# Kernel optimization log

Hardware: AMD Instinct MI355X
Metric: run time of the kernel (lower is better)

Reference implementation:

```python
import jax, jax.numpy as jnp
import numpy as np

BATCH, SEQ, STATE, D_IN, D_OUT = 32, 8192, 128, 128, 128


def setup_inputs() -> dict:
    key = jax.random.key(0)
    k1, k2, k3, k4, k5 = jax.random.split(key, 5)
    A = jnp.tril(jax.random.normal(k1, (STATE, STATE), dtype=jnp.float32) * 0.01)
    B = jax.random.normal(k2, (STATE, D_IN), dtype=jnp.float32) * 0.01
    C = jax.random.normal(k3, (D_OUT, STATE), dtype=jnp.float32) * 0.01
    D = jax.random.normal(k4, (D_OUT, D_IN), dtype=jnp.float32) * 0.01
    u = jax.random.normal(k5, (BATCH, SEQ, D_IN), dtype=jnp.float32)
    return {"u": u, "A": A, "B": B, "C": C, "D": D}


def reference(u, A, B, C, D):
    # u: [b, L, d_in]; A: [S, S] (lower-tri); B: [S, d_in]; C: [d_out, S]; D: [d_out, d_in]
    S = A.shape[0]
    Bu = jnp.einsum('bld,sd->bls', u, B)                      # [b, L, S]
    I_minus_A = jnp.eye(S, dtype=u.dtype) - A                 # [S, S], lower-tri
    # Solve (I - A) x = Bu^T. The matrix is shared across batch and time, so
    # fold (b, L) into one rhs-column axis: one trsm instead of b batched solves.
    rhs = Bu.reshape(-1, S).T                                 # [S, b*L]
    x = jax.scipy.linalg.solve_triangular(I_minus_A, rhs, lower=True)  # [S, b*L]
    x_seq = x.T.reshape(Bu.shape)                             # [b, L, S]
    y = jnp.einsum('bls,os->blo', x_seq, C) + jnp.einsum('bld,od->blo', u, D)
    return y
```

## Files before the change

### kernel.cpp

```cpp
#include <hip/hip_runtime.h>
#include <stdint.h>

typedef __attribute__((ext_vector_type(8))) short bf16x8;
typedef __attribute__((ext_vector_type(4))) float f32x4;

static __device__ __forceinline__ uint16_t f2bf(float f) {
    uint32_t u;
    __builtin_memcpy(&u, &f, 4);
    return (uint16_t)((u + 0x7FFFu + ((u >> 16) & 1u)) >> 16);
}

__global__ __launch_bounds__(128) void k1_solve(const float* __restrict__ Ag,
                                                const float* __restrict__ Bg,
                                                float* __restrict__ X) {
    __shared__ float As[128 * 128];
    const int d = threadIdx.x;
    for (int i = 0; i < 128; ++i) As[i * 128 + d] = Ag[i * 128 + d];
    __syncthreads();

    float x[128];
#pragma unroll
    for (int s = 0; s < 128; ++s) {
        const float* Ar = &As[s * 128];
        float a0 = 0.f, a1 = 0.f, a2 = 0.f, a3 = 0.f;
        const int s4 = s & ~3;
#pragma unroll
        for (int t = 0; t < s4; t += 4) {
            a0 += Ar[t + 0] * x[t + 0];
            a1 += Ar[t + 1] * x[t + 1];
            a2 += Ar[t + 2] * x[t + 2];
            a3 += Ar[t + 3] * x[t + 3];
        }
#pragma unroll
        for (int t = s4; t < s; ++t) a0 += Ar[t] * x[t];
        float num = Bg[s * 128 + d] + ((a0 + a1) + (a2 + a3));
        x[s] = num / (1.0f - Ar[s]);
    }
#pragma unroll
    for (int s = 0; s < 128; ++s) X[s * 128 + d] = x[s];
}

__global__ __launch_bounds__(128) void k2_makeM(const float* __restrict__ X,
                                                const float* __restrict__ Cg,
                                                const float* __restrict__ Dg,
                                                uint16_t* __restrict__ Mfrag) {
    const int o = blockIdx.x;
    const int d = threadIdx.x;
    float a0 = 0.f, a1 = 0.f, a2 = 0.f, a3 = 0.f;
#pragma unroll
    for (int s = 0; s < 128; s += 4) {
        a0 += Cg[o * 128 + s + 0] * X[(s + 0) * 128 + d];
        a1 += Cg[o * 128 + s + 1] * X[(s + 1) * 128 + d];
        a2 += Cg[o * 128 + s + 2] * X[(s + 2) * 128 + d];
        a3 += Cg[o * 128 + s + 3] * X[(s + 3) * 128 + d];
    }
    float m = ((a0 + a1) + (a2 + a3)) + Dg[o * 128 + d];

    const int c = o >> 4, n = o & 15;
    const int t = d >> 5, r = d & 31;
    const int half = r >> 3, j = r & 7;
    const int lane = half * 16 + n;
    const int f = c * 4 + t;
    Mfrag[(f * 64 + lane) * 8 + j] = f2bf(m);
}

__global__ __launch_bounds__(256, 2) void k3_gemm(const float* __restrict__ U,
                                                  const uint16_t* __restrict__ Mfrag,
                                                  float* __restrict__ Y) {
    const int lane = threadIdx.x & 63;
    const int wid  = threadIdx.x >> 6;

    bf16x8 Bfr[8][4];
#pragma unroll
    for (int c = 0; c < 8; ++c)
#pragma unroll
        for (int t = 0; t < 4; ++t)
            Bfr[c][t] = *reinterpret_cast<const bf16x8*>(Mfrag + ((c * 4 + t) * 64 + lane) * 8);

    const int am = lane & 15;
    const int kh = lane >> 4;

#pragma unroll 1
    for (int it = 0; it < 4; ++it) {
        const int rowbase = blockIdx.x * 256 + it * 64 + wid * 16;

        const float* up = U + (size_t)(rowbase + am) * 128 + kh * 8;
        bf16x8 Afr[4];
#pragma unroll
        for (int t = 0; t < 4; ++t) {
            f32x4 lo = *reinterpret_cast<const f32x4*>(up + t * 32);
            f32x4 hi = *reinterpret_cast<const f32x4*>(up + t * 32 + 4);
            bf16x8 a;
#pragma unroll
            for (int j = 0; j < 4; ++j) {
                a[j]     = (short)f2bf(lo[j]);
                a[4 + j] = (short)f2bf(hi[j]);
            }
            Afr[t] = a;
        }

        f32x4 acc[8] = {};
#pragma unroll
        for (int c = 0; c < 8; ++c)
#pragma unroll
            for (int t = 0; t < 4; ++t)
                acc[c] = __builtin_amdgcn_mfma_f32_16x16x32_bf16(Afr[t], Bfr[c][t], acc[c], 0, 0, 0);

        float* yp = Y + (size_t)(rowbase + kh * 4) * 128 + am;
#pragma unroll
        for (int c = 0; c < 8; ++c)
#pragma unroll
            for (int r = 0; r < 4; ++r)
                yp[(size_t)r * 128 + c * 16] = acc[c][r];
    }
}

extern "C" void kernel_launch(void* const* d_in, const int* in_sizes, int n_in,
                              void* d_out, int out_size, void* d_ws, size_t ws_size,
                              hipStream_t stream) {
    const float* u = (const float*)d_in[0];
    const float* A = (const float*)d_in[1];
    const float* B = (const float*)d_in[2];
    const float* C = (const float*)d_in[3];
    const float* D = (const float*)d_in[4];

    float*    X     = (float*)d_ws;
    uint16_t* Mfrag = (uint16_t*)((char*)d_ws + 65536);
    float*    Y     = (float*)d_out;

    hipLaunchKernelGGL(k1_solve, dim3(1),    dim3(128), 0, stream, A, B, X);
    hipLaunchKernelGGL(k2_makeM, dim3(128),  dim3(128), 0, stream, X, C, D, Mfrag);
    hipLaunchKernelGGL(k3_gemm,  dim3(1024), dim3(256), 0, stream, u, Mfrag, Y);
}
```

Measured before the change: 305.6 us.

## Stage M fragments in LDS and raise GEMM occupancy with more blocks

Measured after the change: 302.6 us. About the same (-1.0%).

```diff
diff --git a/kernel.cpp b/kernel.cpp
--- a/kernel.cpp
+++ b/kernel.cpp
@@ -10,9 +10,9 @@
     return (uint16_t)((u + 0x7FFFu + ((u >> 16) & 1u)) >> 16);
 }
 
-__global__ __launch_bounds__(128) void k1_solve(const float* __restrict__ Ag,
-                                                const float* __restrict__ Bg,
-                                                float* __restrict__ X) {
+__global__ __launch_bounds__(128, 1) void k1_solve(const float* __restrict__ Ag,
+                                                   const float* __restrict__ Bg,
+                                                   float* __restrict__ X) {
     __shared__ float As[128 * 128];
     const int d = threadIdx.x;
     for (int i = 0; i < 128; ++i) As[i * 128 + d] = Ag[i * 128 + d];
@@ -26,10 +26,11 @@
         const int s4 = s & ~3;
 #pragma unroll
         for (int t = 0; t < s4; t += 4) {
-            a0 += Ar[t + 0] * x[t + 0];
-            a1 += Ar[t + 1] * x[t + 1];
-            a2 += Ar[t + 2] * x[t + 2];
-            a3 += Ar[t + 3] * x[t + 3];
+            f32x4 av = *reinterpret_cast<const f32x4*>(Ar + t);
+            a0 += av[0] * x[t + 0];
+            a1 += av[1] * x[t + 1];
+            a2 += av[2] * x[t + 2];
+            a3 += av[3] * x[t + 3];
         }
 #pragma unroll
         for (int t = s4; t < s; ++t) a0 += Ar[t] * x[t];
@@ -64,55 +65,57 @@
     Mfrag[(f * 64 + lane) * 8 + j] = f2bf(m);
 }
 
-__global__ __launch_bounds__(256, 2) void k3_gemm(const float* __restrict__ U,
+__global__ __launch_bounds__(256, 4) void k3_gemm(const float* __restrict__ U,
                                                   const uint16_t* __restrict__ Mfrag,
                                                   float* __restrict__ Y) {
+    __shared__ uint16_t Msh[16384];
+    {
+        const uint4* src = reinterpret_cast<const uint4*>(Mfrag);
+        uint4* dst = reinterpret_cast<uint4*>(Msh);
+#pragma unroll
+        for (int i = 0; i < 8; ++i)
+            dst[threadIdx.x + 256 * i] = src[threadIdx.x + 256 * i];
+    }
+    __syncthreads();
+
     const int lane = threadIdx.x & 63;
     const int wid  = threadIdx.x >> 6;
+    const int am = lane & 15;
+    const int kh = lane >> 4;
 
-    bf16x8 Bfr[8][4];
+    const int rowbase = blockIdx.x * 64 + wid * 16;
+
+    const float* up = U + (size_t)(rowbase + am) * 128 + kh * 8;
+    bf16x8 Afr[4];
+#pragma unroll
+    for (int t = 0; t < 4; ++t) {
+        f32x4 lo = *reinterpret_cast<const f32x4*>(up + t * 32);
+        f32x4 hi = *reinterpret_cast<const f32x4*>(up + t * 32 + 4);
+        bf16x8 a;
+#pragma unroll
+        for (int j = 0; j < 4; ++j) {
+            a[j]     = (short)f2bf(lo[j]);
+            a[4 + j] = (short)f2bf(hi[j]);
+        }
+        Afr[t] = a;
+    }
+
+    f32x4 acc[8] = {};
+#pragma unroll
+    for (int c = 0; c < 8; ++c) {
+#pragma unroll
+        for (int t = 0; t < 4; ++t) {
+            bf16x8 b = *reinterpret_cast<const bf16x8*>(Msh + ((c * 4 + t) * 64 + lane) * 8);
+            acc[c] = __builtin_amdgcn_mfma_f32_16x16x32_bf16(Afr[t], b, acc[c], 0, 0, 0);
+        }
+    }
+
+    float* yp = Y + (size_t)(rowbase + kh * 4) * 128 + am;
 #pragma unroll
     for (int c = 0; c < 8; ++c)
 #pragma unroll
-        for (int t = 0; t < 4; ++t)
-            Bfr[c][t] = *reinterpret_cast<const bf16x8*>(Mfrag + ((c * 4 + t) * 64 + lane) * 8);
-
-    const int am = lane & 15;
-    const int kh = lane >> 4;
-
-#pragma unroll 1
-    for (int it = 0; it < 4; ++it) {
-        const int rowbase = blockIdx.x * 256 + it * 64 + wid * 16;
-
-        const float* up = U + (size_t)(rowbase + am) * 128 + kh * 8;
-        bf16x8 Afr[4];
-#pragma unroll
-        for (int t = 0; t < 4; ++t) {
-            f32x4 lo = *reinterpret_cast<const f32x4*>(up + t * 32);
-            f32x4 hi = *reinterpret_cast<const f32x4*>(up + t * 32 + 4);
-            bf16x8 a;
-#pragma unroll
-            for (int j = 0; j < 4; ++j) {
-                a[j]     = (short)f2bf(lo[j]);
-                a[4 + j] = (short)f2bf(hi[j]);
-            }
-            Afr[t] = a;
-        }
-
-        f32x4 acc[8] = {};
-#pragma unroll
-        for (int c = 0; c < 8; ++c)
-#pragma unroll
-            for (int t = 0; t < 4; ++t)
-                acc[c] = __builtin_amdgcn_mfma_f32_16x16x32_bf16(Afr[t], Bfr[c][t], acc[c], 0, 0, 0);
-
-        float* yp = Y + (size_t)(rowbase + kh * 4) * 128 + am;
-#pragma unroll
-        for (int c = 0; c < 8; ++c)
-#pragma unroll
-            for (int r = 0; r < 4; ++r)
-                yp[(size_t)r * 128 + c * 16] = acc[c][r];
-    }
+        for (int r = 0; r < 4; ++r)
+            yp[(size_t)r * 128 + c * 16] = acc[c][r];
 }
 
 extern "C" void kernel_launch(void* const* d_in, const int* in_sizes, int n_in,
@@ -130,5 +133,5 @@
 
     hipLaunchKernelGGL(k1_solve, dim3(1),    dim3(128), 0, stream, A, B, X);
     hipLaunchKernelGGL(k2_makeM, dim3(128),  dim3(128), 0, stream, X, C, D, Mfrag);
-    hipLaunchKernelGGL(k3_gemm,  dim3(1024), dim3(256), 0, stream, u, Mfrag, Y);
+    hipLaunchKernelGGL(k3_gemm,  dim3(4096), dim3(256), 0, stream, u, Mfrag, Y);
 }
```
